# Performance work log

Measured on AMD Instinct MI355X. Metric: run time of the kernel, lower is better.

## Reference

```python
import jax, jax.numpy as jnp
import numpy as np
import math

VOCAB, DIM, N_LAYERS, N_HEADS, SEQ, BATCH = 32000, 768, 4, 12, 2048, 1
HEAD_DIM = DIM // N_HEADS
HIDDEN = int(DIM * 2.66)  # 2042
THETA = 10000.0


def setup_inputs() -> dict:
    key = jax.random.key(0)
    ks = jax.random.split(key, 14)
    s = 0.02
    return {
        "tokens": jax.random.randint(ks[0], (BATCH, SEQ), 0, VOCAB),
        "emb": jax.random.normal(ks[1], (VOCAB, DIM), jnp.float32) * s,
        "wq": jax.random.normal(ks[2], (N_LAYERS, DIM, DIM), jnp.float32) * s,
        "wk": jax.random.normal(ks[3], (N_LAYERS, DIM, DIM), jnp.float32) * s,
        "wv": jax.random.normal(ks[4], (N_LAYERS, DIM, DIM), jnp.float32) * s,
        "wo": jax.random.normal(ks[5], (N_LAYERS, DIM, DIM), jnp.float32) * s,
        "w1": jax.random.normal(ks[6], (N_LAYERS, HIDDEN, DIM), jnp.float32) * s,
        "w2": jax.random.normal(ks[7], (N_LAYERS, DIM, HIDDEN), jnp.float32) * s,
        "w3": jax.random.normal(ks[8], (N_LAYERS, HIDDEN, DIM), jnp.float32) * s,
        "attn_norm_w": jnp.ones((N_LAYERS, DIM), jnp.float32),
        "ffn_norm_w": jnp.ones((N_LAYERS, DIM), jnp.float32),
        "norm_w": jnp.ones((DIM,), jnp.float32),
        "out_w": jax.random.normal(ks[9], (VOCAB, DIM), jnp.float32) * s,
    }


def rmsnorm(x, w, eps=1e-6):
    return x * jax.lax.rsqrt(jnp.mean(x * x, axis=-1, keepdims=True) + eps) * w


def rope_tables(seqlen):
    freqs = 1.0 / (THETA ** (jnp.arange(0, HEAD_DIM, 2, dtype=jnp.float32) / HEAD_DIM))
    ang = jnp.arange(seqlen, dtype=jnp.float32)[:, None] * freqs[None, :]  # [S, hd/2]
    return jnp.cos(ang)[None, :, None, :], jnp.sin(ang)[None, :, None, :]


def apply_rope(x, cos, sin):
    # x: [B,S,H,hd]; complex rotation on consecutive pairs
    xr = x.reshape(*x.shape[:-1], HEAD_DIM // 2, 2)
    a, b = xr[..., 0], xr[..., 1]
    out = jnp.stack([a * cos - b * sin, a * sin + b * cos], axis=-1)
    return out.reshape(x.shape)


def reference(tokens, emb, wq, wk, wv, wo, w1, w2, w3, attn_norm_w, ffn_norm_w, norm_w, out_w):
    B, S = tokens.shape
    h = emb[tokens]  # [B,S,D]
    cos, sin = rope_tables(S)
    mask = jnp.triu(jnp.full((S, S), -jnp.inf, jnp.float32), k=1)  # causal
    scale = 1.0 / math.sqrt(HEAD_DIM)
    for i in range(N_LAYERS):
        x = rmsnorm(h, attn_norm_w[i])
        q = (x @ wq[i].T).reshape(B, S, N_HEADS, HEAD_DIM)
        k = (x @ wk[i].T).reshape(B, S, N_HEADS, HEAD_DIM)
        v = (x @ wv[i].T).reshape(B, S, N_HEADS, HEAD_DIM)
        q = apply_rope(q, cos, sin)
        k = apply_rope(k, cos, sin)
        scores = jnp.einsum("bqhd,bkhd->bhqk", q, k) * scale + mask
        p = jax.nn.softmax(scores, axis=-1)
        o = jnp.einsum("bhqk,bkhd->bqhd", p, v).reshape(B, S, DIM)
        h = h + o @ wo[i].T
        y = rmsnorm(h, ffn_norm_w[i])
        h = h + (jax.nn.silu(y @ w1[i].T) * (y @ w3[i].T)) @ w2[i].T
    h = rmsnorm(h, norm_w)
    logits = h @ out_w.T  # [B,S,V]
    return logits
```

## Files before the change

kernel.cpp:

```cpp
#include <hip/hip_runtime.h>
#include <math.h>

typedef unsigned int uint32;
typedef unsigned short ushort_t;

typedef __attribute__((ext_vector_type(8))) short short8;
typedef __attribute__((ext_vector_type(4))) float floatx4;

#define SEQL 2048
#define DIMC 768
#define NHEAD 12
#define HDIM 64
#define HIDV 2042
#define HIDP 2048
#define NVOCAB 32000
#define QKS 1536
#define QSZ (DIMC*DIMC)
#define PSZ (HIDP*DIMC)
#define W2SRC (DIMC*HIDV)

__device__ __forceinline__ ushort_t f2bf(float f) {
    uint32 u = __float_as_uint(f);
    u += 0x7FFFu + ((u >> 16) & 1u);
    return (ushort_t)(u >> 16);
}
__device__ __forceinline__ float bf2f(ushort_t h) {
    return __uint_as_float(((uint32)h) << 16);
}

union Frag { short8 s8; uint32 u[4]; ushort_t us[8]; };

#define GLOAD_LDS16(g, l) \
    __builtin_amdgcn_global_load_lds((const __attribute__((address_space(1))) void*)(g), \
                                     (__attribute__((address_space(3))) void*)(l), 16, 0, 0)

template<int BM, int BN, int OUTMODE>
__global__ __launch_bounds__(256)
void gemm_lds_kernel(const ushort_t* __restrict__ A, int lda,
                     const ushort_t* __restrict__ B, int ldb,
                     void* __restrict__ C, int ldc, int K)
{
    constexpr int WTM = BM / 32;
    constexpr int WTN = BN / 32;
    __shared__ __align__(16) ushort_t As[2][BM * 32];
    __shared__ __align__(16) ushort_t Bs[2][BN * 32];

    const int tid = threadIdx.x;
    const int nwg  = gridDim.x * gridDim.y;
    const int lid0 = blockIdx.y * gridDim.x + blockIdx.x;
    const int lid  = (lid0 & 7) * (nwg >> 3) + (lid0 >> 3);
    const int bx = lid % gridDim.x;
    const int by = lid / gridDim.x;

    const int wid = tid >> 6, lane = tid & 63;
    const int wm = wid & 1, wn = wid >> 1;
    const int r = lane & 15, quad = lane >> 4;
    const int m0 = bx * BM;
    const int n0 = by * BN;

    floatx4 acc[WTM][WTN];
#pragma unroll
    for (int i = 0; i < WTM; ++i)
#pragma unroll
        for (int j = 0; j < WTN; ++j) acc[i][j] = (floatx4){0.f, 0.f, 0.f, 0.f};

    const int row_a = tid >> 2;
    const int col8  = (tid & 3) * 8;
    const ushort_t* gA = A + (size_t)(m0 + row_a) * lda + col8;
    const ushort_t* gB = B + (size_t)(n0 + row_a) * ldb + col8;

    auto stage = [&](int buf, int k0) {
        GLOAD_LDS16(gA + k0, &As[buf][(size_t)tid * 8]);
        if (BM == 128) GLOAD_LDS16(gA + (size_t)64 * lda + k0, &As[buf][(size_t)(tid + 256) * 8]);
        GLOAD_LDS16(gB + k0, &Bs[buf][(size_t)tid * 8]);
        if (BN == 128) GLOAD_LDS16(gB + (size_t)64 * ldb + k0, &Bs[buf][(size_t)(tid + 256) * 8]);
    };

    stage(0, 0);
    __syncthreads();
    int buf = 0;
    for (int k0 = 0; k0 < K; k0 += 32) {
        if (k0 + 32 < K) stage(buf ^ 1, k0 + 32);
        const ushort_t* pa = &As[buf][(wm * (BM / 2) + r) * 32 + quad * 8];
        const ushort_t* pb = &Bs[buf][(wn * (BN / 2) + r) * 32 + quad * 8];
        short8 af[WTM], bf[WTN];
#pragma unroll
        for (int i = 0; i < WTM; ++i) af[i] = *(const short8*)(pa + i * 16 * 32);
#pragma unroll
        for (int j = 0; j < WTN; ++j) bf[j] = *(const short8*)(pb + j * 16 * 32);
#pragma unroll
        for (int i = 0; i < WTM; ++i)
#pragma unroll
            for (int j = 0; j < WTN; ++j)
                acc[i][j] = __builtin_amdgcn_mfma_f32_16x16x32_bf16(af[i], bf[j], acc[i][j], 0, 0, 0);
        __syncthreads();
        buf ^= 1;
    }

#pragma unroll
    for (int i = 0; i < WTM; ++i) {
        const int row = m0 + wm * (BM / 2) + i * 16 + quad * 4;
#pragma unroll
        for (int j = 0; j < WTN; ++j) {
            const int col = n0 + wn * (BN / 2) + j * 16 + r;
#pragma unroll
            for (int t = 0; t < 4; ++t) {
                const size_t off = (size_t)(row + t) * ldc + col;
                const float v = acc[i][j][t];
                if (OUTMODE == 2)      ((float*)C)[off] += v;
                else if (OUTMODE == 1) ((ushort_t*)C)[off] = f2bf(v);
                else                   ((float*)C)[off] = v;
            }
        }
    }
}

__global__ __launch_bounds__(256)
void rmsnorm_kernel(const float* __restrict__ x, const float* __restrict__ g,
                    ushort_t* __restrict__ out)
{
    const int w = threadIdx.x >> 6, lane = threadIdx.x & 63;
    const int row = blockIdx.x * 4 + w;
    const float* xr = x + (size_t)row * DIMC;
    float4 a = *(const float4*)(xr + lane * 4);
    float4 b = *(const float4*)(xr + 256 + lane * 4);
    float4 c = *(const float4*)(xr + 512 + lane * 4);
    float ss = a.x*a.x + a.y*a.y + a.z*a.z + a.w*a.w
             + b.x*b.x + b.y*b.y + b.z*b.z + b.w*b.w
             + c.x*c.x + c.y*c.y + c.z*c.z + c.w*c.w;
#pragma unroll
    for (int off = 32; off > 0; off >>= 1) ss += __shfl_xor(ss, off, 64);
    const float inv = rsqrtf(ss * (1.0f / DIMC) + 1e-6f);
    float4 ga = *(const float4*)(g + lane * 4);
    float4 gb = *(const float4*)(g + 256 + lane * 4);
    float4 gc = *(const float4*)(g + 512 + lane * 4);
    ushort_t* orow = out + (size_t)row * DIMC;
    *(ushort4*)(orow + lane * 4)       = make_ushort4(f2bf(a.x*inv*ga.x), f2bf(a.y*inv*ga.y), f2bf(a.z*inv*ga.z), f2bf(a.w*inv*ga.w));
    *(ushort4*)(orow + 256 + lane * 4) = make_ushort4(f2bf(b.x*inv*gb.x), f2bf(b.y*inv*gb.y), f2bf(b.z*inv*gb.z), f2bf(b.w*inv*gb.w));
    *(ushort4*)(orow + 512 + lane * 4) = make_ushort4(f2bf(c.x*inv*gc.x), f2bf(c.y*inv*gc.y), f2bf(c.z*inv*gc.z), f2bf(c.w*inv*gc.w));
}

__global__ __launch_bounds__(256)
void rope_kernel(ushort_t* __restrict__ x)
{
    const int idx = blockIdx.x * 256 + threadIdx.x;
    const int j = idx & 31;
    const int h = (idx >> 5) % 24;
    const int s = idx / 768;
    const float freq = expf(-0.28782313662425574f * (float)j);
    const float ang = (float)s * freq;
    const float sn = sinf(ang), cs = cosf(ang);
    ushort_t* p = x + (size_t)s * QKS + h * HDIM + 2 * j;
    const float a = bf2f(p[0]), b = bf2f(p[1]);
    p[0] = f2bf(a * cs - b * sn);
    p[1] = f2bf(a * sn + b * cs);
}

__global__ __launch_bounds__(256)
void attn_mfma_kernel(const ushort_t* __restrict__ Q, const ushort_t* __restrict__ K,
                      const ushort_t* __restrict__ VT, ushort_t* __restrict__ O,
                      int qks)
{
    __shared__ __align__(16) ushort_t Ks[2][128 * 64];
    __shared__ __align__(16) ushort_t Vs[2][64 * 128];

    const int tid = threadIdx.x;
    const int w = tid >> 6, lane = tid & 63;
    const int r = lane & 15, quad = lane >> 4;
    const int hb = blockIdx.y * HDIM;
    const int bx = 31 - (int)blockIdx.x;
    const int qb = bx * 64 + w * 16;
    const int nit = (bx + 2) >> 1;

    const int krow = tid >> 3;
    const int kcol = ((tid & 7) ^ (krow & 7)) << 3;
    const int vrow = tid >> 4;
    const int vcol = (((tid & 15) ^ (vrow & 7))) << 3;
    const int swz = (r & 7) << 4;

    Frag bq[2];
    {
        const ushort_t* qp = Q + (size_t)(qb + r) * qks + hb + quad * 8;
#pragma unroll
        for (int fi = 0; fi < 2; ++fi) {
            Frag t; t.s8 = *(const short8*)(qp + fi * 32);
#pragma unroll
            for (int e = 0; e < 8; ++e) t.us[e] = f2bf(bf2f(t.us[e]) * 0.125f);
            bq[fi] = t;
        }
    }

    floatx4 o[4];
#pragma unroll
    for (int dg = 0; dg < 4; ++dg) o[dg] = (floatx4){0.f, 0.f, 0.f, 0.f};
    float m = -INFINITY, l = 0.f;

    auto stage = [&](int buf, int kc) {
        const ushort_t* kg = K + (size_t)(kc + krow) * qks + hb + kcol;
        GLOAD_LDS16(kg,                      &Ks[buf][(size_t)tid * 8]);
        GLOAD_LDS16(kg + (size_t)32 * qks,   &Ks[buf][(size_t)(tid + 256) * 8]);
        GLOAD_LDS16(kg + (size_t)64 * qks,   &Ks[buf][(size_t)(tid + 512) * 8]);
        GLOAD_LDS16(kg + (size_t)96 * qks,   &Ks[buf][(size_t)(tid + 768) * 8]);
        const ushort_t* vg = VT + (size_t)(hb + vrow) * SEQL + kc + vcol;
        GLOAD_LDS16(vg,                      &Vs[buf][(size_t)tid * 8]);
        GLOAD_LDS16(vg + (size_t)16 * SEQL,  &Vs[buf][(size_t)(tid + 256) * 8]);
        GLOAD_LDS16(vg + (size_t)32 * SEQL,  &Vs[buf][(size_t)(tid + 512) * 8]);
        GLOAD_LDS16(vg + (size_t)48 * SEQL,  &Vs[buf][(size_t)(tid + 768) * 8]);
    };

    stage(0, 0);
    __syncthreads();

    for (int it = 0; it < nit; ++it) {
        const int buf = it & 1;
        const int kc = it * 128;
        if (it + 1 < nit) stage(buf ^ 1, kc + 128);

        const char* ksb = (const char*)Ks[buf];
        const char* vsb = (const char*)Vs[buf];

        floatx4 st[8];
        __builtin_amdgcn_s_setprio(1);
#pragma unroll
        for (int s = 0; s < 8; ++s) {
            st[s] = (floatx4){0.f, 0.f, 0.f, 0.f};
#pragma unroll
            for (int f = 0; f < 2; ++f) {
                const int lb = (s * 16 + r) * 128 + ((f * 64 + quad * 16) ^ swz);
                const short8 a = *(const short8*)(ksb + lb);
                st[s] = __builtin_amdgcn_mfma_f32_16x16x32_bf16(a, bq[f].s8, st[s], 0, 0, 0);
            }
        }
        __builtin_amdgcn_s_setprio(0);

        if (it == nit - 1) {
            const int q = qb + r;
#pragma unroll
            for (int s = 0; s < 8; ++s)
#pragma unroll
                for (int tt = 0; tt < 4; ++tt)
                    if (kc + s * 16 + quad * 4 + tt > q) st[s][tt] = -INFINITY;
        }

        float vm = -INFINITY;
#pragma unroll
        for (int s = 0; s < 8; ++s)
            vm = fmaxf(vm, fmaxf(fmaxf(st[s][0], st[s][1]), fmaxf(st[s][2], st[s][3])));
        vm = fmaxf(vm, __shfl_xor(vm, 16, 64));
        vm = fmaxf(vm, __shfl_xor(vm, 32, 64));
        const float mnew = fmaxf(m, vm);
        const float alpha = __expf(m - mnew);
        float ps = 0.f;
#pragma unroll
        for (int s = 0; s < 8; ++s)
#pragma unroll
            for (int tt = 0; tt < 4; ++tt) {
                st[s][tt] = __expf(st[s][tt] - mnew);
                ps += st[s][tt];
            }
        ps += __shfl_xor(ps, 16, 64);
        ps += __shfl_xor(ps, 32, 64);
        l = l * alpha + ps;
        m = mnew;

        Frag ap[4];
#pragma unroll
        for (int ks = 0; ks < 4; ++ks) {
            ap[ks].u[0] = (uint32)f2bf(st[2*ks][0])   | ((uint32)f2bf(st[2*ks][1])   << 16);
            ap[ks].u[1] = (uint32)f2bf(st[2*ks][2])   | ((uint32)f2bf(st[2*ks][3])   << 16);
            ap[ks].u[2] = (uint32)f2bf(st[2*ks+1][0]) | ((uint32)f2bf(st[2*ks+1][1]) << 16);
            ap[ks].u[3] = (uint32)f2bf(st[2*ks+1][2]) | ((uint32)f2bf(st[2*ks+1][3]) << 16);
        }

        __builtin_amdgcn_s_setprio(1);
#pragma unroll
        for (int dg = 0; dg < 4; ++dg) {
            const int rowb = (dg * 16 + r) * 256;
            o[dg] *= alpha;
#pragma unroll
            for (int ks = 0; ks < 4; ++ks) {
                Frag av;
                *(uint2*)&av.u[0] = *(const uint2*)(vsb + rowb + ((ks * 64 + quad * 8) ^ swz));
                *(uint2*)&av.u[2] = *(const uint2*)(vsb + rowb + ((ks * 64 + 32 + quad * 8) ^ swz));
                o[dg] = __builtin_amdgcn_mfma_f32_16x16x32_bf16(av.s8, ap[ks].s8, o[dg], 0, 0, 0);
            }
        }
        __builtin_amdgcn_s_setprio(0);

        __syncthreads();
    }

    const float inv = 1.0f / l;
    ushort_t* op = O + (size_t)(qb + r) * DIMC + hb + quad * 4;
#pragma unroll
    for (int dg = 0; dg < 4; ++dg) {
        uint2 pkd;
        pkd.x = (uint32)f2bf(o[dg][0] * inv) | ((uint32)f2bf(o[dg][1] * inv) << 16);
        pkd.y = (uint32)f2bf(o[dg][2] * inv) | ((uint32)f2bf(o[dg][3] * inv) << 16);
        *(uint2*)(op + dg * 16) = pkd;
    }
}

__global__ __launch_bounds__(256)
void silu_mul_kernel(const ushort_t* __restrict__ y13, ushort_t* __restrict__ hs)
{
    const int idx = blockIdx.x * 256 + threadIdx.x;
    const int s = idx >> 8;
    const int c = (idx & 255) * 8;
    const ushort_t* row = y13 + (size_t)s * 4096;
    short8 a8 = *(const short8*)(row + c);
    short8 b8 = *(const short8*)(row + 2048 + c);
    ushort_t ov[8];
#pragma unroll
    for (int e = 0; e < 8; ++e) {
        const float a = bf2f((ushort_t)a8[e]);
        const float b = bf2f((ushort_t)b8[e]);
        ov[e] = f2bf(a / (1.f + __expf(-a)) * b);
    }
    short8 pk;
#pragma unroll
    for (int e = 0; e < 8; ++e) pk[e] = (short)ov[e];
    *(short8*)(hs + (size_t)s * HIDP + c) = pk;
}

__global__ __launch_bounds__(256)
void embed_kernel(const int* __restrict__ tok, const float* __restrict__ emb,
                  float* __restrict__ h)
{
    const int idx = blockIdx.x * 256 + threadIdx.x;
    const int s = idx / 192, c = (idx % 192) * 4;
    const int t = tok[s];
    *(float4*)(h + (size_t)s * DIMC + c) = *(const float4*)(emb + (size_t)t * DIMC + c);
}

__global__ __launch_bounds__(256)
void conv_layer_kernel(const float* __restrict__ wq, const float* __restrict__ wk,
                       const float* __restrict__ wv, const float* __restrict__ wo,
                       const float* __restrict__ w1, const float* __restrict__ w2,
                       const float* __restrict__ w3,
                       ushort_t* __restrict__ wqb, ushort_t* __restrict__ wkb,
                       ushort_t* __restrict__ wvb, ushort_t* __restrict__ wob,
                       ushort_t* __restrict__ w1p, ushort_t* __restrict__ w3p,
                       ushort_t* __restrict__ w2p)
{
    int idx = blockIdx.x * 256 + threadIdx.x;
    if (idx < 4 * QSZ) {
        const int m = idx / QSZ, i = idx - m * QSZ;
        const float* s = (m == 0) ? wq : (m == 1) ? wk : (m == 2) ? wv : wo;
        ushort_t*   d = (m == 0) ? wqb : (m == 1) ? wkb : (m == 2) ? wvb : wob;
        d[i] = f2bf(s[i]);
        return;
    }
    idx -= 4 * QSZ;
    if (idx < PSZ) {
        const int n = idx / DIMC, kk = idx - n * DIMC;
        w1p[idx] = (n < HIDV) ? f2bf(w1[(size_t)n * DIMC + kk]) : (ushort_t)0;
        return;
    }
    idx -= PSZ;
    if (idx < PSZ) {
        const int n = idx / DIMC, kk = idx - n * DIMC;
        w3p[idx] = (n < HIDV) ? f2bf(w3[(size_t)n * DIMC + kk]) : (ushort_t)0;
        return;
    }
    idx -= PSZ;
    if (idx < PSZ) {
        const int n = idx >> 11, kk = idx & 2047;
        w2p[idx] = (kk < HIDV) ? f2bf(w2[(size_t)n * HIDV + kk]) : (ushort_t)0;
        return;
    }
}

__global__ __launch_bounds__(256)
void conv_outw_kernel(const float* __restrict__ src, ushort_t* __restrict__ dst)
{
    const size_t idx = (size_t)(blockIdx.x * 256 + threadIdx.x);
    float4 a = *(const float4*)(src + idx * 4);
    *(ushort4*)(dst + idx * 4) = make_ushort4(f2bf(a.x), f2bf(a.y), f2bf(a.z), f2bf(a.w));
}

extern "C" void kernel_launch(void* const* d_in, const int* in_sizes, int n_in,
                              void* d_out, int out_size, void* d_ws, size_t ws_size,
                              hipStream_t stream)
{
    const int*   tok  = (const int*)d_in[0];
    const float* emb  = (const float*)d_in[1];
    const float* wq   = (const float*)d_in[2];
    const float* wk   = (const float*)d_in[3];
    const float* wv   = (const float*)d_in[4];
    const float* wo   = (const float*)d_in[5];
    const float* w1   = (const float*)d_in[6];
    const float* w2   = (const float*)d_in[7];
    const float* w3   = (const float*)d_in[8];
    const float* anw  = (const float*)d_in[9];
    const float* fnw  = (const float*)d_in[10];
    const float* nw   = (const float*)d_in[11];
    const float* outw = (const float*)d_in[12];
    float* out = (float*)d_out;
    (void)in_sizes; (void)n_in; (void)out_size; (void)ws_size;

    char* p = (char*)d_ws;
    auto alloc = [&](size_t bytes) { char* r = p; p += (bytes + 255) & ~(size_t)255; return r; };
    float*    H   = (float*)   alloc((size_t)SEQL * DIMC * 4);
    ushort_t* XN  = (ushort_t*)alloc((size_t)SEQL * DIMC * 2);
    ushort_t* YN  = (ushort_t*)alloc((size_t)SEQL * DIMC * 2);
    ushort_t* WQB = (ushort_t*)alloc((size_t)QSZ * 2);
    ushort_t* WKB = (ushort_t*)alloc((size_t)QSZ * 2);
    ushort_t* WVB = (ushort_t*)alloc((size_t)QSZ * 2);
    ushort_t* WOB = (ushort_t*)alloc((size_t)QSZ * 2);
    ushort_t* W1P = (ushort_t*)alloc((size_t)PSZ * 2);
    ushort_t* W3P = (ushort_t*)alloc((size_t)PSZ * 2);
    ushort_t* W2P = (ushort_t*)alloc((size_t)PSZ * 2);
    ushort_t* QKB = (ushort_t*)alloc((size_t)SEQL * QKS * 2);
    ushort_t* VTG = (ushort_t*)alloc((size_t)SEQL * DIMC * 2);
    ushort_t* AO  = (ushort_t*)alloc((size_t)SEQL * DIMC * 2);
    ushort_t* Y13 = (ushort_t*)alloc((size_t)SEQL * 4096 * 2);
    ushort_t* HS  = (ushort_t*)alloc((size_t)SEQL * HIDP * 2);
    ushort_t* OUTWB = QKB;

    embed_kernel<<<1536, 256, 0, stream>>>(tok, emb, H);

    for (int l = 0; l < 4; ++l) {
        conv_layer_kernel<<<27648, 256, 0, stream>>>(
            wq + (size_t)l * QSZ, wk + (size_t)l * QSZ, wv + (size_t)l * QSZ, wo + (size_t)l * QSZ,
            w1 + (size_t)l * W2SRC, w2 + (size_t)l * W2SRC, w3 + (size_t)l * W2SRC,
            WQB, WKB, WVB, WOB, W1P, W3P, W2P);

        rmsnorm_kernel<<<512, 256, 0, stream>>>(H, anw + (size_t)l * DIMC, XN);

        gemm_lds_kernel<128,128,1><<<dim3(16,12), 256, 0, stream>>>(XN, DIMC, WQB, DIMC, QKB, QKS, DIMC);
        gemm_lds_kernel<64,128,1><<<dim3(12,16), 256, 0, stream>>>(WVB, DIMC, XN, DIMC, VTG, SEQL, DIMC);

        rope_kernel<<<6144, 256, 0, stream>>>(QKB);

        attn_mfma_kernel<<<dim3(32, NHEAD), 256, 0, stream>>>(QKB, QKB + 768, VTG, AO, QKS);

        gemm_lds_kernel<128,64,2><<<dim3(16,12), 256, 0, stream>>>(AO, DIMC, WOB, DIMC, H, DIMC, DIMC);

        rmsnorm_kernel<<<512, 256, 0, stream>>>(H, fnw + (size_t)l * DIMC, YN);

        gemm_lds_kernel<128,128,1><<<dim3(16,32), 256, 0, stream>>>(YN, DIMC, W1P, DIMC, Y13, 4096, DIMC);

        silu_mul_kernel<<<2048, 256, 0, stream>>>(Y13, HS);

        gemm_lds_kernel<128,64,2><<<dim3(16,12), 256, 0, stream>>>(HS, HIDP, W2P, HIDP, H, DIMC, HIDP);
    }

    rmsnorm_kernel<<<512, 256, 0, stream>>>(H, nw, XN);
    conv_outw_kernel<<<24000, 256, 0, stream>>>(outw, OUTWB);
    gemm_lds_kernel<128,128,0><<<dim3(16,250), 256, 0, stream>>>(XN, DIMC, OUTWB, DIMC, out, NVOCAB, DIMC);
}
```

Baseline: 1.305 ms.

## Fuse RoPE and SiLU-mul into GEMM epilogues, merge QKV launches, convert weights once

```diff
diff --git a/kernel.cpp b/kernel.cpp
--- a/kernel.cpp
+++ b/kernel.cpp
@@ -18,6 +18,7 @@
 #define QSZ (DIMC*DIMC)
 #define PSZ (HIDP*DIMC)
 #define W2SRC (DIMC*HIDV)
+#define LSTR (4*QSZ + 3*PSZ)
 
 __device__ __forceinline__ ushort_t f2bf(float f) {
     uint32 u = __float_as_uint(f);
@@ -97,19 +98,137 @@
         buf ^= 1;
     }
 
-#pragma unroll
-    for (int i = 0; i < WTM; ++i) {
-        const int row = m0 + wm * (BM / 2) + i * 16 + quad * 4;
-#pragma unroll
-        for (int j = 0; j < WTN; ++j) {
-            const int col = n0 + wn * (BN / 2) + j * 16 + r;
-#pragma unroll
-            for (int t = 0; t < 4; ++t) {
-                const size_t off = (size_t)(row + t) * ldc + col;
-                const float v = acc[i][j][t];
-                if (OUTMODE == 2)      ((float*)C)[off] += v;
-                else if (OUTMODE == 1) ((ushort_t*)C)[off] = f2bf(v);
-                else                   ((float*)C)[off] = v;
+    if (OUTMODE == 4) {
+#pragma unroll
+        for (int i = 0; i < WTM; ++i) {
+            const int row = m0 + wm * (BM / 2) + i * 16 + quad * 4;
+#pragma unroll
+            for (int jp = 0; jp < WTN / 2; ++jp) {
+                const int col = n0 / 2 + wn * (BN / 4) + jp * 16 + r;
+#pragma unroll
+                for (int t = 0; t < 4; ++t) {
+                    const float a = acc[i][2 * jp][t];
+                    const float b = acc[i][2 * jp + 1][t];
+                    ((ushort_t*)C)[(size_t)(row + t) * ldc + col] =
+                        f2bf(a / (1.f + __expf(-a)) * b);
+                }
+            }
+        }
+    } else {
+#pragma unroll
+        for (int i = 0; i < WTM; ++i) {
+            const int row = m0 + wm * (BM / 2) + i * 16 + quad * 4;
+#pragma unroll
+            for (int j = 0; j < WTN; ++j) {
+                const int col = n0 + wn * (BN / 2) + j * 16 + r;
+#pragma unroll
+                for (int t = 0; t < 4; ++t) {
+                    const size_t off = (size_t)(row + t) * ldc + col;
+                    const float v = acc[i][j][t];
+                    if (OUTMODE == 2)      ((float*)C)[off] += v;
+                    else if (OUTMODE == 1) ((ushort_t*)C)[off] = f2bf(v);
+                    else                   ((float*)C)[off] = v;
+                }
+            }
+        }
+    }
+}
+
+__global__ __launch_bounds__(256)
+void gemm_qkvt_kernel(const ushort_t* __restrict__ XN_,
+                      const ushort_t* __restrict__ WQK,
+                      const ushort_t* __restrict__ WVB_,
+                      ushort_t* __restrict__ QKB_,
+                      ushort_t* __restrict__ VTG_)
+{
+    __shared__ __align__(16) ushort_t As[2][128 * 32];
+    __shared__ __align__(16) ushort_t Bs[2][128 * 32];
+
+    const int tid = threadIdx.x;
+    const int lid0 = blockIdx.x;
+    const int lid  = (lid0 & 7) * 36 + (lid0 >> 3);
+    int job, bx, by;
+    if (lid < 192) { job = 0; bx = lid & 15; by = lid >> 4; }
+    else { const int t2 = lid - 192; job = 1; bx = t2 % 6; by = t2 / 6; }
+
+    const ushort_t* A = job ? WVB_ : XN_;
+    const ushort_t* B = job ? XN_  : WQK;
+
+    const int wid = tid >> 6, lane = tid & 63;
+    const int wm = wid & 1, wn = wid >> 1;
+    const int r = lane & 15, quad = lane >> 4;
+    const int m0 = bx * 128;
+    const int n0 = by * 128;
+
+    floatx4 acc[4][4];
+#pragma unroll
+    for (int i = 0; i < 4; ++i)
+#pragma unroll
+        for (int j = 0; j < 4; ++j) acc[i][j] = (floatx4){0.f, 0.f, 0.f, 0.f};
+
+    const int row_a = tid >> 2;
+    const int col8  = (tid & 3) * 8;
+    const ushort_t* gA = A + (size_t)(m0 + row_a) * DIMC + col8;
+    const ushort_t* gB = B + (size_t)(n0 + row_a) * DIMC + col8;
+
+    auto stage = [&](int buf, int k0) {
+        GLOAD_LDS16(gA + k0,                      &As[buf][(size_t)tid * 8]);
+        GLOAD_LDS16(gA + (size_t)64 * DIMC + k0,  &As[buf][(size_t)(tid + 256) * 8]);
+        GLOAD_LDS16(gB + k0,                      &Bs[buf][(size_t)tid * 8]);
+        GLOAD_LDS16(gB + (size_t)64 * DIMC + k0,  &Bs[buf][(size_t)(tid + 256) * 8]);
+    };
+
+    stage(0, 0);
+    __syncthreads();
+    int buf = 0;
+    for (int k0 = 0; k0 < DIMC; k0 += 32) {
+        if (k0 + 32 < DIMC) stage(buf ^ 1, k0 + 32);
+        const ushort_t* pa = &As[buf][(wm * 64 + r) * 32 + quad * 8];
+        const ushort_t* pb = &Bs[buf][(wn * 64 + r) * 32 + quad * 8];
+        short8 af[4], bf[4];
+#pragma unroll
+        for (int i = 0; i < 4; ++i) af[i] = *(const short8*)(pa + i * 16 * 32);
+#pragma unroll
+        for (int j = 0; j < 4; ++j) bf[j] = *(const short8*)(pb + j * 16 * 32);
+#pragma unroll
+        for (int i = 0; i < 4; ++i)
+#pragma unroll
+            for (int j = 0; j < 4; ++j)
+                acc[i][j] = __builtin_amdgcn_mfma_f32_16x16x32_bf16(af[i], bf[j], acc[i][j], 0, 0, 0);
+        __syncthreads();
+        buf ^= 1;
+    }
+
+    if (job == 1) {
+#pragma unroll
+        for (int i = 0; i < 4; ++i) {
+            const int row = m0 + wm * 64 + i * 16 + quad * 4;
+#pragma unroll
+            for (int j = 0; j < 4; ++j) {
+                const int col = n0 + wn * 64 + j * 16 + r;
+#pragma unroll
+                for (int t = 0; t < 4; ++t)
+                    VTG_[(size_t)(row + t) * SEQL + col] = f2bf(acc[i][j][t]);
+            }
+        }
+    } else {
+#pragma unroll
+        for (int j = 0; j < 4; ++j) {
+            const int dh = j * 16 + r;
+            const float freq = __expf(-0.28782313662425574f * (float)(dh >> 1));
+            const int col = n0 + wn * 64 + dh;
+#pragma unroll
+            for (int i = 0; i < 4; ++i) {
+                const int row = m0 + wm * 64 + i * 16 + quad * 4;
+#pragma unroll
+                for (int t = 0; t < 4; ++t) {
+                    const float ang = (float)(row + t) * freq;
+                    const float cs = cosf(ang), sn = sinf(ang);
+                    const float v  = acc[i][j][t];
+                    const float pv = __shfl_xor(v, 1, 64);
+                    const float ov = (r & 1) ? (pv * sn + v * cs) : (v * cs - pv * sn);
+                    QKB_[(size_t)(row + t) * QKS + col] = f2bf(ov);
+                }
             }
         }
     }
@@ -138,22 +257,6 @@
     *(ushort4*)(orow + lane * 4)       = make_ushort4(f2bf(a.x*inv*ga.x), f2bf(a.y*inv*ga.y), f2bf(a.z*inv*ga.z), f2bf(a.w*inv*ga.w));
     *(ushort4*)(orow + 256 + lane * 4) = make_ushort4(f2bf(b.x*inv*gb.x), f2bf(b.y*inv*gb.y), f2bf(b.z*inv*gb.z), f2bf(b.w*inv*gb.w));
     *(ushort4*)(orow + 512 + lane * 4) = make_ushort4(f2bf(c.x*inv*gc.x), f2bf(c.y*inv*gc.y), f2bf(c.z*inv*gc.z), f2bf(c.w*inv*gc.w));
-}
-
-__global__ __launch_bounds__(256)
-void rope_kernel(ushort_t* __restrict__ x)
-{
-    const int idx = blockIdx.x * 256 + threadIdx.x;
-    const int j = idx & 31;
-    const int h = (idx >> 5) % 24;
-    const int s = idx / 768;
-    const float freq = expf(-0.28782313662425574f * (float)j);
-    const float ang = (float)s * freq;
-    const float sn = sinf(ang), cs = cosf(ang);
-    ushort_t* p = x + (size_t)s * QKS + h * HDIM + 2 * j;
-    const float a = bf2f(p[0]), b = bf2f(p[1]);
-    p[0] = f2bf(a * cs - b * sn);
-    p[1] = f2bf(a * sn + b * cs);
 }
 
 __global__ __launch_bounds__(256)
@@ -302,28 +405,6 @@
 }
 
 __global__ __launch_bounds__(256)
-void silu_mul_kernel(const ushort_t* __restrict__ y13, ushort_t* __restrict__ hs)
-{
-    const int idx = blockIdx.x * 256 + threadIdx.x;
-    const int s = idx >> 8;
-    const int c = (idx & 255) * 8;
-    const ushort_t* row = y13 + (size_t)s * 4096;
-    short8 a8 = *(const short8*)(row + c);
-    short8 b8 = *(const short8*)(row + 2048 + c);
-    ushort_t ov[8];
-#pragma unroll
-    for (int e = 0; e < 8; ++e) {
-        const float a = bf2f((ushort_t)a8[e]);
-        const float b = bf2f((ushort_t)b8[e]);
-        ov[e] = f2bf(a / (1.f + __expf(-a)) * b);
-    }
-    short8 pk;
-#pragma unroll
-    for (int e = 0; e < 8; ++e) pk[e] = (short)ov[e];
-    *(short8*)(hs + (size_t)s * HIDP + c) = pk;
-}
-
-__global__ __launch_bounds__(256)
 void embed_kernel(const int* __restrict__ tok, const float* __restrict__ emb,
                   float* __restrict__ h)
 {
@@ -334,41 +415,32 @@
 }
 
 __global__ __launch_bounds__(256)
-void conv_layer_kernel(const float* __restrict__ wq, const float* __restrict__ wk,
-                       const float* __restrict__ wv, const float* __restrict__ wo,
-                       const float* __restrict__ w1, const float* __restrict__ w2,
-                       const float* __restrict__ w3,
-                       ushort_t* __restrict__ wqb, ushort_t* __restrict__ wkb,
-                       ushort_t* __restrict__ wvb, ushort_t* __restrict__ wob,
-                       ushort_t* __restrict__ w1p, ushort_t* __restrict__ w3p,
-                       ushort_t* __restrict__ w2p)
-{
-    int idx = blockIdx.x * 256 + threadIdx.x;
-    if (idx < 4 * QSZ) {
-        const int m = idx / QSZ, i = idx - m * QSZ;
-        const float* s = (m == 0) ? wq : (m == 1) ? wk : (m == 2) ? wv : wo;
-        ushort_t*   d = (m == 0) ? wqb : (m == 1) ? wkb : (m == 2) ? wvb : wob;
-        d[i] = f2bf(s[i]);
-        return;
-    }
-    idx -= 4 * QSZ;
-    if (idx < PSZ) {
-        const int n = idx / DIMC, kk = idx - n * DIMC;
-        w1p[idx] = (n < HIDV) ? f2bf(w1[(size_t)n * DIMC + kk]) : (ushort_t)0;
-        return;
-    }
-    idx -= PSZ;
-    if (idx < PSZ) {
-        const int n = idx / DIMC, kk = idx - n * DIMC;
-        w3p[idx] = (n < HIDV) ? f2bf(w3[(size_t)n * DIMC + kk]) : (ushort_t)0;
-        return;
-    }
-    idx -= PSZ;
-    if (idx < PSZ) {
-        const int n = idx >> 11, kk = idx & 2047;
-        w2p[idx] = (kk < HIDV) ? f2bf(w2[(size_t)n * HIDV + kk]) : (ushort_t)0;
-        return;
-    }
+void conv_all_kernel(const float* __restrict__ wq, const float* __restrict__ wk,
+                     const float* __restrict__ wv, const float* __restrict__ wo,
+                     const float* __restrict__ w1, const float* __restrict__ w2,
+                     const float* __restrict__ w3, ushort_t* __restrict__ wall)
+{
+    const int l = blockIdx.y;
+    const int j = blockIdx.x * 256 + threadIdx.x;
+    float v;
+    if (j < 2 * QSZ) {
+        v = (j < QSZ) ? wq[(size_t)l * QSZ + j] : wk[(size_t)l * QSZ + j - QSZ];
+    } else if (j < 3 * QSZ) {
+        v = wv[(size_t)l * QSZ + j - 2 * QSZ];
+    } else if (j < 4 * QSZ) {
+        v = wo[(size_t)l * QSZ + j - 3 * QSZ];
+    } else if (j < 4 * QSZ + 2 * PSZ) {
+        const int jj = j - 4 * QSZ;
+        const int row = jj / DIMC, kk = jj - row * DIMC;
+        const int hp = (row >> 5) * 16 + (row & 15);
+        const int src = (row >> 4) & 1;
+        v = (hp < HIDV) ? (src ? w3 : w1)[(size_t)l * W2SRC + (size_t)hp * DIMC + kk] : 0.f;
+    } else {
+        const int jj = j - 4 * QSZ - 2 * PSZ;
+        const int n = jj >> 11, kk = jj & 2047;
+        v = (kk < HIDV) ? w2[(size_t)l * W2SRC + (size_t)n * HIDV + kk] : 0.f;
+    }
+    wall[(size_t)l * LSTR + j] = f2bf(v);
 }
 
 __global__ __launch_bounds__(256)
@@ -401,37 +473,30 @@
 
     char* p = (char*)d_ws;
     auto alloc = [&](size_t bytes) { char* r = p; p += (bytes + 255) & ~(size_t)255; return r; };
-    float*    H   = (float*)   alloc((size_t)SEQL * DIMC * 4);
-    ushort_t* XN  = (ushort_t*)alloc((size_t)SEQL * DIMC * 2);
-    ushort_t* YN  = (ushort_t*)alloc((size_t)SEQL * DIMC * 2);
-    ushort_t* WQB = (ushort_t*)alloc((size_t)QSZ * 2);
-    ushort_t* WKB = (ushort_t*)alloc((size_t)QSZ * 2);
-    ushort_t* WVB = (ushort_t*)alloc((size_t)QSZ * 2);
-    ushort_t* WOB = (ushort_t*)alloc((size_t)QSZ * 2);
-    ushort_t* W1P = (ushort_t*)alloc((size_t)PSZ * 2);
-    ushort_t* W3P = (ushort_t*)alloc((size_t)PSZ * 2);
-    ushort_t* W2P = (ushort_t*)alloc((size_t)PSZ * 2);
-    ushort_t* QKB = (ushort_t*)alloc((size_t)SEQL * QKS * 2);
-    ushort_t* VTG = (ushort_t*)alloc((size_t)SEQL * DIMC * 2);
-    ushort_t* AO  = (ushort_t*)alloc((size_t)SEQL * DIMC * 2);
-    ushort_t* Y13 = (ushort_t*)alloc((size_t)SEQL * 4096 * 2);
-    ushort_t* HS  = (ushort_t*)alloc((size_t)SEQL * HIDP * 2);
-    ushort_t* OUTWB = QKB;
+    float*    H    = (float*)   alloc((size_t)SEQL * DIMC * 4);
+    ushort_t* XN   = (ushort_t*)alloc((size_t)SEQL * DIMC * 2);
+    ushort_t* YN   = (ushort_t*)alloc((size_t)SEQL * DIMC * 2);
+    ushort_t* WALL = (ushort_t*)alloc((size_t)4 * LSTR * 2);
+    ushort_t* QKB  = (ushort_t*)alloc((size_t)SEQL * QKS * 2);
+    ushort_t* VTG  = (ushort_t*)alloc((size_t)SEQL * DIMC * 2);
+    ushort_t* AO   = (ushort_t*)alloc((size_t)SEQL * DIMC * 2);
+    ushort_t* HS   = (ushort_t*)alloc((size_t)SEQL * HIDP * 2);
+    ushort_t* OUTWB= (ushort_t*)alloc((size_t)NVOCAB * DIMC * 2);
 
     embed_kernel<<<1536, 256, 0, stream>>>(tok, emb, H);
+    conv_all_kernel<<<dim3(LSTR / 256, 4), 256, 0, stream>>>(wq, wk, wv, wo, w1, w2, w3, WALL);
 
     for (int l = 0; l < 4; ++l) {
-        conv_layer_kernel<<<27648, 256, 0, stream>>>(
-            wq + (size_t)l * QSZ, wk + (size_t)l * QSZ, wv + (size_t)l * QSZ, wo + (size_t)l * QSZ,
-            w1 + (size_t)l * W2SRC, w2 + (size_t)l * W2SRC, w3 + (size_t)l * W2SRC,
-            WQB, WKB, WVB, WOB, W1P, W3P, W2P);
+        ushort_t* WL  = WALL + (size_t)l * LSTR;
+        ushort_t* WQK = WL;
+        ushort_t* WVB = WL + 2 * QSZ;
+        ushort_t* WOB = WL + 3 * QSZ;
+        ushort_t* W13 = WL + 4 * QSZ;
+        ushort_t* W2P = WL + 4 * QSZ + 2 * PSZ;
 
         rmsnorm_kernel<<<512, 256, 0, stream>>>(H, anw + (size_t)l * DIMC, XN);
 
-        gemm_lds_kernel<128,128,1><<<dim3(16,12), 256, 0, stream>>>(XN, DIMC, WQB, DIMC, QKB, QKS, DIMC);
-        gemm_lds_kernel<64,128,1><<<dim3(12,16), 256, 0, stream>>>(WVB, DIMC, XN, DIMC, VTG, SEQL, DIMC);
-
-        rope_kernel<<<6144, 256, 0, stream>>>(QKB);
+        gemm_qkvt_kernel<<<288, 256, 0, stream>>>(XN, WQK, WVB, QKB, VTG);
 
         attn_mfma_kernel<<<dim3(32, NHEAD), 256, 0, stream>>>(QKB, QKB + 768, VTG, AO, QKS);
 
@@ -439,9 +504,7 @@
 
         rmsnorm_kernel<<<512, 256, 0, stream>>>(H, fnw + (size_t)l * DIMC, YN);
 
-        gemm_lds_kernel<128,128,1><<<dim3(16,32), 256, 0, stream>>>(YN, DIMC, W1P, DIMC, Y13, 4096, DIMC);
-
-        silu_mul_kernel<<<2048, 256, 0, stream>>>(Y13, HS);
+        gemm_lds_kernel<128,128,4><<<dim3(16,32), 256, 0, stream>>>(YN, DIMC, W13, DIMC, HS, HIDP, DIMC);
 
         gemm_lds_kernel<128,64,2><<<dim3(16,12), 256, 0, stream>>>(HS, HIDP, W2P, HIDP, H, DIMC, HIDP);
     }
```

Measured after the change: 1.922 ms. 47.3% more time.
